# Optimization experiments

Hardware: AMD Instinct MI355X
Metric: run time of the kernel (lower is better)

Reference implementation:

```python
import jax, jax.numpy as jnp
import numpy as np

N = 4096          # batch of anchors
D = 128           # embedding dim
M = 4             # instances per class (balanced batch) -> 3 positives per anchor
MARGIN = 1.0
INF = jnp.float32(1e30)


def setup_inputs() -> dict:
    key = jax.random.key(0)
    inputs = jax.random.normal(key, (N, D), dtype=jnp.float32)
    targets = (jnp.arange(N, dtype=jnp.int32) // M).astype(jnp.int32)
    return {"inputs": inputs, "targets": targets}


def _forward(inputs, targets, key):
    n = inputs.shape[0]
    k_pos = M - 1            # positives per anchor (and multinomial draw count)
    k_neg = n - M            # negatives per anchor

    # euclidean_dist: ||xi||^2 + ||xj||^2 - 2 xi.xj, clamped and sqrt'ed
    sq = jnp.sum(inputs * inputs, axis=1)
    dist = sq[:, None] + sq[None, :] - 2.0 * (inputs @ inputs.T)
    dist = jnp.sqrt(jnp.clip(dist, 1e-12, None))

    same = targets[:, None] == targets[None, :]
    eye = jnp.eye(n, dtype=bool)
    pos_mask = same & ~eye
    neg_mask = ~same

    # balanced batch -> exactly k_pos positives / k_neg negatives per row;
    # push non-members to +inf and sort (original sorts pos/neg pairs anyway)
    pos_sorted = jnp.sort(jnp.where(pos_mask, dist, INF), axis=1)[:, :k_pos]  # [n, 3]
    neg_sorted = jnp.sort(jnp.where(neg_mask, dist, INF), axis=1)[:, :k_neg]  # [n, n-M]

    pos3 = pos_sorted[:, :3]  # pos_pair[:3]

    # GaussDistribution over the (sorted) negative row
    neg_mean = jnp.mean(neg_sorted, axis=1, keepdims=True)
    neg_std = jnp.sqrt(jnp.mean((neg_sorted - neg_mean) ** 2, axis=1, keepdims=True))
    # prob = exp((x-mean)^2 / (2 std^2)); use log-weights for Gumbel-top-k
    log_prob = (neg_sorted - neg_mean) ** 2 / (2.0 * neg_std ** 2)

    # multinomial without replacement == top-k of log_prob + Gumbel noise
    g = jax.random.gumbel(key, neg_sorted.shape, dtype=jnp.float32)
    _, idx = jax.lax.top_k(log_prob + g, k_pos)                 # [n, 3]
    sampled = jnp.take_along_axis(neg_sorted, idx, axis=1)      # [n, 3]

    # masked_select(neg_pair < pos_pair[-1] + 0.05) -> boolean keep mask
    kept = sampled < (pos3[:, -1:] + 0.05)
    cnt = jnp.sum(kept, axis=1)
    any_kept = cnt > 0

    # pos_loss = 0.5*mean(log(1+exp(-2*(margin - pos))))
    pos_loss = 0.5 * jnp.mean(jax.nn.softplus(-2.0 * (MARGIN - pos3)), axis=1)
    # neg_loss = 0.05*mean over kept of log(1+exp(20*(margin - neg)))
    neg_terms = jax.nn.softplus(20.0 * (MARGIN - sampled))
    neg_loss = 0.05 * jnp.sum(jnp.where(kept, neg_terms, 0.0), axis=1) / jnp.maximum(cnt, 1)

    row_loss = jnp.where(any_kept, pos_loss + neg_loss, 0.0)
    loss = jnp.sum(row_loss) / n

    # err: pos_pair[0] < neg_pair[0] - 0.1 (first kept sampled negative)
    first_idx = jnp.argmax(kept, axis=1)
    neg0 = jnp.take_along_axis(sampled, first_idx[:, None], axis=1)[:, 0]
    err = jnp.sum((any_kept & (pos3[:, 0] < neg0 - 0.1)).astype(jnp.float32))
    prec = 1.0 - err / n

    pos_d = jnp.mean(pos_sorted)
    neg_d = jnp.mean(neg_sorted)
    return loss, prec, pos_d, neg_d


def reference(inputs, targets):
    key = jax.random.key(42)  # fixed sampling key (torch.multinomial analogue)
    return _forward(inputs, targets, key)
```

## Files before the change

### kernel.cpp

```cpp
#include <hip/hip_runtime.h>
#include <stdint.h>

#define NROW 4096
#define NDIM 128
#define KNEG 4092
#define INF_VAL 1e30f
#define BUCKETS 2048
#define GTOT ((size_t)NROW * (size_t)KNEG)
#define DISTBLKS 1024
#define DSTR 68

typedef __attribute__((ext_vector_type(8))) short short8;
typedef __attribute__((ext_vector_type(4))) float f32x4;

__device__ __forceinline__ uint32_t rotl32(uint32_t v, int d) {
  return __builtin_rotateleft32(v, (unsigned)d);
}

__device__ __forceinline__ void threefry2x32(uint32_t x0, uint32_t x1,
                                             uint32_t& y0, uint32_t& y1) {
  const uint32_t k0 = 0u, k1 = 42u;
  const uint32_t k2 = 0x1BD11BDAu ^ k0 ^ k1;
  uint32_t v0 = x0 + k0, v1 = x1 + k1;
#define TF_R(r) v0 += v1; v1 = rotl32(v1, r); v1 ^= v0;
  TF_R(13) TF_R(15) TF_R(26) TF_R(6)
  v0 += k1; v1 += k2 + 1u;
  TF_R(17) TF_R(29) TF_R(16) TF_R(24)
  v0 += k2; v1 += k0 + 2u;
  TF_R(13) TF_R(15) TF_R(26) TF_R(6)
  v0 += k0; v1 += k1 + 3u;
  TF_R(17) TF_R(29) TF_R(16) TF_R(24)
  v0 += k1; v1 += k2 + 4u;
  TF_R(13) TF_R(15) TF_R(26) TF_R(6)
  v0 += k2; v1 += k0 + 5u;
#undef TF_R
  y0 = v0; y1 = v1;
}

__device__ __forceinline__ float gumbel_ref(uint32_t f) {
  uint32_t y0, y1;
  threefry2x32(0u, f, y0, y1);
  uint32_t m = y1 >> 9;
  float fm = (float)m;
  float nl = fmaf(-0.69314718f, __log2f(fm), 15.942385f);
  if (m == 0u) nl = 87.33655f;
  return -0.69314718f * __log2f(nl);
}

__device__ __forceinline__ float softplus_ref(float x) {
  return fmaxf(x, 0.0f) + log1pf(expf(-fabsf(x)));
}

__device__ __forceinline__ ushort f2h(float f) {
  _Float16 h = (_Float16)f;
  return *(ushort*)&h;
}
__device__ __forceinline__ float h2f(ushort u) {
  _Float16 h = *(_Float16*)&u;
  return (float)h;
}
__device__ __forceinline__ float bf2f(ushort u) {
  return __uint_as_float(((uint32_t)u) << 16);
}
__device__ __forceinline__ ushort f2bf(float f) {
  uint32_t u = __float_as_uint(f);
  u += 0x7fffu + ((u >> 16) & 1u);
  return (ushort)(u >> 16);
}

__device__ __forceinline__ int bucket_code(ushort code) {
  return min(max((int)code - 0x4000, 0), BUCKETS - 1);
}

__global__ __launch_bounds__(64) void prep_kernel(const float* __restrict__ X,
                                                  float* __restrict__ sq,
                                                  ushort* __restrict__ Xbf) {
  int i = blockIdx.x;
  int lane = threadIdx.x;
  float2 v = ((const float2*)(X + (size_t)i * NDIM))[lane];
  float s = v.x * v.x + v.y * v.y;
  for (int o = 32; o > 0; o >>= 1) s += __shfl_down(s, o);
  if (lane == 0) sq[i] = s;
  ushort2 h;
  h.x = f2bf(v.x);
  h.y = f2bf(v.y);
  ((ushort2*)(Xbf + (size_t)i * NDIM))[lane] = h;
}

__global__ __launch_bounds__(256) void dist_gumbel(const ushort* __restrict__ Xbf,
                                                   const float* __restrict__ sq,
                                                   ushort* __restrict__ distb,
                                                   ushort* __restrict__ gh) {
  __shared__ ushort Als[128 * DSTR];
  __shared__ ushort Bls[128 * DSTR];
  const int tid = threadIdx.x;
  const int bi = blockIdx.x >> 5, bj = blockIdx.x & 31;
  const int wave = tid >> 6, lane = tid & 63;
  const int q = lane >> 4, ln = lane & 15;
  const ushort* Ag = Xbf + (size_t)bi * 128 * NDIM;
  const ushort* Bg = Xbf + (size_t)bj * 128 * NDIM;

  f32x4 acc[8][2];
#pragma unroll
  for (int mt = 0; mt < 8; ++mt)
#pragma unroll
    for (int nt = 0; nt < 2; ++nt) acc[mt][nt] = (f32x4){0.f, 0.f, 0.f, 0.f};

  for (int kh = 0; kh < 2; ++kh) {
    if (kh) __syncthreads();
#pragma unroll
    for (int t = 0; t < 4; ++t) {
      int c = tid + 256 * t;
      int r = c >> 3, k8 = (c & 7) << 3;
      *(short8*)&Als[r * DSTR + k8] =
          *(const short8*)(Ag + (size_t)r * NDIM + kh * 64 + k8);
      *(short8*)&Bls[r * DSTR + k8] =
          *(const short8*)(Bg + (size_t)r * NDIM + kh * 64 + k8);
    }
    __syncthreads();
#pragma unroll
    for (int k0 = 0; k0 < 64; k0 += 32) {
      int kf = k0 + q * 8;
      short8 a[8], b[2];
#pragma unroll
      for (int mt = 0; mt < 8; ++mt)
        a[mt] = *(const short8*)&Als[(mt * 16 + ln) * DSTR + kf];
#pragma unroll
      for (int nt = 0; nt < 2; ++nt)
        b[nt] = *(const short8*)&Bls[(wave * 32 + 2 * ln + nt) * DSTR + kf];
#pragma unroll
      for (int mt = 0; mt < 8; ++mt)
#pragma unroll
        for (int nt = 0; nt < 2; ++nt)
          acc[mt][nt] = __builtin_amdgcn_mfma_f32_16x16x32_bf16(
              a[mt], b[nt], acc[mt][nt], 0, 0, 0);
    }
  }

  const int jcol = bj * 128 + wave * 32 + 2 * ln;
  float sqj0 = sq[jcol], sqj1 = sq[jcol + 1];
#pragma unroll
  for (int mt = 0; mt < 8; ++mt) {
    int ibase = bi * 128 + mt * 16 + q * 4;
#pragma unroll
    for (int r = 0; r < 4; ++r) {
      int i = ibase + r;
      float sqi = sq[i];
      float dx = sqrtf(fmaxf(sqi + sqj0 - 2.0f * acc[mt][0][r], 1e-12f));
      float dy = sqrtf(fmaxf(sqi + sqj1 - 2.0f * acc[mt][1][r], 1e-12f));
      uint32_t pack = ((uint32_t)f2bf(dy) << 16) | (uint32_t)f2bf(dx);
      *(uint32_t*)(distb + (size_t)i * NROW + jcol) = pack;
    }
  }

  if (gh) {
    uint32_t b0 = (uint32_t)blockIdx.x * 16368u;
#pragma unroll
    for (int t = 0; t < 16; ++t) {
      int c = tid + 256 * t;
      if (c < 4092) {
        uint32_t f0 = b0 + (uint32_t)c * 4u;
        ushort4 h;
        h.x = f2h(gumbel_ref(f0 + 0u));
        h.y = f2h(gumbel_ref(f0 + 1u));
        h.z = f2h(gumbel_ref(f0 + 2u));
        h.w = f2h(gumbel_ref(f0 + 3u));
        *(ushort4*)(gh + f0) = h;
      }
    }
  }
}

__global__ __launch_bounds__(256) void row_kernel(const ushort* __restrict__ distb,
                                                  const ushort* __restrict__ Gh,
                                                  float4* __restrict__ part) {
  __shared__ alignas(16) ushort sortc[NROW];
  __shared__ alignas(16) int base[BUCKETS];
  __shared__ float wredf[8];
  __shared__ int wtot[4];
  __shared__ float s_pos[3];
  __shared__ float s_sel[3];

  float* cscore = (float*)base;
  float* cx     = (float*)base + 768;
  int*   crank  = (int*)sortc;
  float* redf   = (float*)((char*)sortc + 3072);
  int*   redi   = (int*)((char*)sortc + 4096);
  int*   redi2  = (int*)((char*)sortc + 5120);

  const int i = blockIdx.x;
  const int tid = threadIdx.x;
  const int lane = tid & 63, wid = tid >> 6;
  const ushort* row = distb + (size_t)i * NROW;
  const int gbase = i & ~3;

  {
    int4* b4 = (int4*)base;
    b4[tid] = (int4){0, 0, 0, 0};
    b4[tid + 256] = (int4){0, 0, 0, 0};
  }

  ushort cd[16];
  float x[16];
  {
    short8 r0 = *(const short8*)(row + tid * 16);
    short8 r1 = *(const short8*)(row + tid * 16 + 8);
#pragma unroll
    for (int k = 0; k < 8; ++k) {
      cd[k] = (ushort)r0[k];     x[k] = bf2f(cd[k]);
      cd[8 + k] = (ushort)r1[k]; x[8 + k] = bf2f(cd[8 + k]);
    }
  }

  if (tid == (gbase >> 4)) {
    float p[3]; int np = 0;
#pragma unroll
    for (int qq = 0; qq < 4; ++qq) {
      int j = gbase + qq;
      if (j != i) p[np++] = x[j & 15];
    }
    float a = p[0], b = p[1], c = p[2], t_;
    if (a > b) { t_ = a; a = b; b = t_; }
    if (b > c) { t_ = b; b = c; c = t_; }
    if (a > b) { t_ = a; a = b; b = t_; }
    s_pos[0] = a; s_pos[1] = b; s_pos[2] = c;
  }

#pragma unroll
  for (int qq = 0; qq < 16; ++qq) {
    int j = tid * 16 + qq;
    if ((j >> 2) == (i >> 2)) { x[qq] = INF_VAL; cd[qq] = 0x7F80u; }
  }
  __syncthreads();

  int bkt[16];
  int ord[16];
  float ls = 0.f;
#pragma unroll
  for (int qq = 0; qq < 16; ++qq) {
    bkt[qq] = bucket_code(cd[qq]);
    ord[qq] = atomicAdd(&base[bkt[qq]], 1);
    if (x[qq] < 1e29f) ls += x[qq];
  }
  for (int o = 32; o > 0; o >>= 1) ls += __shfl_down(ls, o);
  if (lane == 0) wredf[wid] = ls;
  __syncthreads();
  const float negsum = wredf[0] + wredf[1] + wredf[2] + wredf[3];
  const float mean = negsum / (float)KNEG;

  int c8[8]; int lsum = 0;
#pragma unroll
  for (int qq = 0; qq < 8; ++qq) {
    int t_ = base[tid * 8 + qq];
    c8[qq] = lsum; lsum += t_;
  }
  float ls2 = 0.f;
#pragma unroll
  for (int qq = 0; qq < 16; ++qq)
    if (x[qq] < 1e29f) { float z = x[qq] - mean; ls2 += z * z; }
  int incl = lsum;
  for (int off = 1; off < 64; off <<= 1) {
    int o = __shfl_up(incl, off);
    if (lane >= off) incl += o;
  }
  for (int o = 32; o > 0; o >>= 1) ls2 += __shfl_down(ls2, o);
  if (lane == 63) wtot[wid] = incl;
  if (lane == 0) wredf[4 + wid] = ls2;
  __syncthreads();
  const float var = (wredf[4] + wredf[5] + wredf[6] + wredf[7]) / (float)KNEG;
  const float stdv = sqrtf(var);
  const float rdenom = __frcp_rn(2.0f * stdv * stdv);
  int excl = incl - lsum;
#pragma unroll
  for (int w = 0; w < 4; ++w) if (w < wid) excl += wtot[w];
#pragma unroll
  for (int qq = 0; qq < 8; ++qq) base[tid * 8 + qq] = excl + c8[qq];
  __syncthreads();

#pragma unroll
  for (int qq = 0; qq < 16; ++qq) {
    int p = base[bkt[qq]] + ord[qq];
    sortc[p] = cd[qq];
  }
  __syncthreads();

  const uint32_t fbase = (uint32_t)i * (uint32_t)KNEG;
  const ushort* grow = Gh ? (Gh + fbase) : nullptr;
  ushort gcode[16];
  if (grow) {
#pragma unroll
    for (int qq = 0; qq < 16; ++qq) gcode[qq] = grow[tid + 256 * qq];
  }

  float t0s = -1e38f, t1s = -1e38f, t2s = -1e38f;
  int   t0r = 0x7fffffff, t1r = 0x7fffffff, t2r = 0x7fffffff;
  float t0x = 0.f, t1x = 0.f, t2x = 0.f;
#pragma unroll
  for (int qq = 0; qq < 16; ++qq) {
    int p = tid + 256 * qq;
    float xv = bf2f(sortc[p]);
    if (p < KNEG) {
      float z = xv - mean;
      float gv = grow ? h2f(gcode[qq]) : gumbel_ref(fbase + (uint32_t)p);
      float sv = fmaf(z * z, rdenom, gv);
      if (sv > t2s || (sv == t2s && p < t2r)) {
        t2s = sv; t2r = p; t2x = xv;
        if (t2s > t1s || (t2s == t1s && t2r < t1r)) {
          float ts = t1s; int tr = t1r; float tx = t1x;
          t1s = t2s; t1r = t2r; t1x = t2x; t2s = ts; t2r = tr; t2x = tx;
        }
        if (t1s > t0s || (t1s == t0s && t1r < t0r)) {
          float ts = t0s; int tr = t0r; float tx = t0x;
          t0s = t1s; t0r = t1r; t0x = t1x; t1s = ts; t1r = tr; t1x = tx;
        }
      }
    }
  }
  __syncthreads();

  cscore[tid * 3 + 0] = t0s; crank[tid * 3 + 0] = t0r; cx[tid * 3 + 0] = t0x;
  cscore[tid * 3 + 1] = t1s; crank[tid * 3 + 1] = t1r; cx[tid * 3 + 1] = t1x;
  cscore[tid * 3 + 2] = t2s; crank[tid * 3 + 2] = t2r; cx[tid * 3 + 2] = t2x;
  __syncthreads();

  for (int t = 0; t < 3; ++t) {
    float bs = -1e38f; int br = 0x7fffffff; int bidx = 0;
    for (int k = tid; k < 768; k += 256) {
      float s_ = cscore[k]; int r_ = crank[k];
      if (s_ > bs || (s_ == bs && r_ < br)) { bs = s_; br = r_; bidx = k; }
    }
    redf[tid] = bs; redi[tid] = br; redi2[tid] = bidx;
    __syncthreads();
    if (tid < 64) {
      float s0_ = redf[tid]; int r0_ = redi[tid]; int i0_ = redi2[tid];
#pragma unroll
      for (int o = 64; o < 256; o += 64) {
        float s1 = redf[tid + o]; int r1 = redi[tid + o];
        if (s1 > s0_ || (s1 == s0_ && r1 < r0_)) {
          s0_ = s1; r0_ = r1; i0_ = redi2[tid + o];
        }
      }
      for (int off = 32; off > 0; off >>= 1) {
        float s1 = __shfl_down(s0_, off);
        int r1 = __shfl_down(r0_, off);
        int i1 = __shfl_down(i0_, off);
        if (s1 > s0_ || (s1 == s0_ && r1 < r0_)) { s0_ = s1; r0_ = r1; i0_ = i1; }
      }
      if (tid == 0) { s_sel[t] = cx[i0_]; cscore[i0_] = -1e38f; }
    }
    __syncthreads();
  }

  if (tid == 0) {
    float p0 = s_pos[0], p1 = s_pos[1], p2 = s_pos[2];
    float thr = p2 + 0.05f;
    float samp[3]; bool kept[3]; int cnt = 0;
#pragma unroll
    for (int t = 0; t < 3; ++t) {
      samp[t] = s_sel[t];
      kept[t] = samp[t] < thr;
      cnt += kept[t] ? 1 : 0;
    }
    bool any = cnt > 0;
    float pos_loss = 0.5f *
        (softplus_ref(-2.0f * (1.0f - p0)) + softplus_ref(-2.0f * (1.0f - p1)) +
         softplus_ref(-2.0f * (1.0f - p2))) / 3.0f;
    float nsum = 0.0f;
#pragma unroll
    for (int t = 0; t < 3; ++t)
      if (kept[t]) nsum += softplus_ref(20.0f * (1.0f - samp[t]));
    float neg_loss = 0.05f * nsum / (float)(cnt > 0 ? cnt : 1);
    float row_loss = any ? (pos_loss + neg_loss) : 0.0f;
    int first = kept[0] ? 0 : (kept[1] ? 1 : (kept[2] ? 2 : 0));
    float neg0 = samp[first];
    float errv = (any && (p0 < neg0 - 0.1f)) ? 1.0f : 0.0f;
    float4 pr;
    pr.x = row_loss; pr.y = errv; pr.z = p0 + p1 + p2; pr.w = negsum;
    part[i] = pr;
  }
}

__global__ __launch_bounds__(256) void reduce_kernel(const float4* __restrict__ part,
                                                     float* __restrict__ out) {
  __shared__ double wsum[4][4];
  const int tid = threadIdx.x;
  const int lane = tid & 63, wid = tid >> 6;
  double s0 = 0.0, s1 = 0.0, s2 = 0.0, s3 = 0.0;
  for (int k = tid; k < NROW; k += 256) {
    float4 v = part[k];
    s0 += (double)v.x; s1 += (double)v.y; s2 += (double)v.z; s3 += (double)v.w;
  }
  for (int o = 32; o > 0; o >>= 1) {
    s0 += __shfl_down(s0, o); s1 += __shfl_down(s1, o);
    s2 += __shfl_down(s2, o); s3 += __shfl_down(s3, o);
  }
  if (lane == 0) {
    wsum[wid][0] = s0; wsum[wid][1] = s1; wsum[wid][2] = s2; wsum[wid][3] = s3;
  }
  __syncthreads();
  if (tid == 0) {
    double a0 = wsum[0][0] + wsum[1][0] + wsum[2][0] + wsum[3][0];
    double a1 = wsum[0][1] + wsum[1][1] + wsum[2][1] + wsum[3][1];
    double a2 = wsum[0][2] + wsum[1][2] + wsum[2][2] + wsum[3][2];
    double a3 = wsum[0][3] + wsum[1][3] + wsum[2][3] + wsum[3][3];
    out[0] = (float)(a0 / (double)NROW);
    out[1] = (float)(1.0 - a1 / (double)NROW);
    out[2] = (float)(a2 / ((double)NROW * 3.0));
    out[3] = (float)(a3 / ((double)NROW * (double)KNEG));
  }
}

extern "C" void kernel_launch(void* const* d_in, const int* in_sizes, int n_in,
                              void* d_out, int out_size, void* d_ws, size_t ws_size,
                              hipStream_t stream) {
  (void)in_sizes; (void)n_in; (void)out_size;
  const float* X = (const float*)d_in[0];
  float* out = (float*)d_out;
  char* ws = (char*)d_ws;

  ushort* distb = (ushort*)ws;
  size_t off = (size_t)NROW * NROW * sizeof(ushort);
  float* sq = (float*)(ws + off);            off += NROW * sizeof(float);
  ushort* Xbf = (ushort*)(ws + off);         off += (size_t)NROW * NDIM * sizeof(ushort);
  float4* part = (float4*)(ws + off);        off += (size_t)NROW * sizeof(float4);
  ushort* Gh = nullptr;
  if (ws_size >= off + GTOT * sizeof(ushort)) Gh = (ushort*)(ws + off);

  prep_kernel<<<NROW, 64, 0, stream>>>(X, sq, Xbf);
  dist_gumbel<<<DISTBLKS, 256, 0, stream>>>(Xbf, sq, distb, Gh);
  row_kernel<<<NROW, 256, 0, stream>>>(distb, Gh, part);
  reduce_kernel<<<1, 256, 0, stream>>>(part, out);
}
```

Baseline: 172.0 us.

## Skip scatter pass in row counting sort, fuse final reduce via last-block

The row kernel no longer scatters bucket codes into a sorted shared array. Each element keeps its bucket and in-bucket offset packed in registers, so its sorted rank comes from the prefix-summed bucket starts and is used directly to index Gumbel noise that is staged once into shared memory. The histogram is split into two copies, one per half-wave, to reduce atomic contention. The separate reduce kernel is folded into the row kernel through a last-block-done atomic counter, and prep now runs four rows per 256-thread block. Together these remove one barrier and scatter pass, one launch and some LDS traffic, at the cost of extra shared memory and atomic fences.

```diff
diff --git a/kernel.cpp b/kernel.cpp
--- a/kernel.cpp
+++ b/kernel.cpp
@@ -72,11 +72,13 @@
   return min(max((int)code - 0x4000, 0), BUCKETS - 1);
 }
 
-__global__ __launch_bounds__(64) void prep_kernel(const float* __restrict__ X,
-                                                  float* __restrict__ sq,
-                                                  ushort* __restrict__ Xbf) {
-  int i = blockIdx.x;
-  int lane = threadIdx.x;
+__global__ __launch_bounds__(256) void prep_kernel(const float* __restrict__ X,
+                                                   float* __restrict__ sq,
+                                                   ushort* __restrict__ Xbf,
+                                                   uint32_t* __restrict__ cnt) {
+  const int tid = threadIdx.x;
+  const int lane = tid & 63;
+  const int i = (blockIdx.x << 2) + (tid >> 6);
   float2 v = ((const float2*)(X + (size_t)i * NDIM))[lane];
   float s = v.x * v.x + v.y * v.y;
   for (int o = 32; o > 0; o >>= 1) s += __shfl_down(s, o);
@@ -85,6 +87,7 @@
   h.x = f2bf(v.x);
   h.y = f2bf(v.y);
   ((ushort2*)(Xbf + (size_t)i * NDIM))[lane] = h;
+  if (blockIdx.x == 0 && tid == 0) *cnt = 0u;
 }
 
 __global__ __launch_bounds__(256) void dist_gumbel(const ushort* __restrict__ Xbf,
@@ -173,20 +176,27 @@
 
 __global__ __launch_bounds__(256) void row_kernel(const ushort* __restrict__ distb,
                                                   const ushort* __restrict__ Gh,
-                                                  float4* __restrict__ part) {
-  __shared__ alignas(16) ushort sortc[NROW];
-  __shared__ alignas(16) int base[BUCKETS];
+                                                  float4* __restrict__ part,
+                                                  uint32_t* __restrict__ cnt,
+                                                  float* __restrict__ out) {
+  __shared__ alignas(16) int baseA[BUCKETS];
+  __shared__ alignas(16) int baseB_raw[BUCKETS + 16];
+  __shared__ alignas(16) ushort Gls[4096];
   __shared__ float wredf[8];
   __shared__ int wtot[4];
   __shared__ float s_pos[3];
   __shared__ float s_sel[3];
-
-  float* cscore = (float*)base;
-  float* cx     = (float*)base + 768;
-  int*   crank  = (int*)sortc;
-  float* redf   = (float*)((char*)sortc + 3072);
-  int*   redi   = (int*)((char*)sortc + 4096);
-  int*   redi2  = (int*)((char*)sortc + 5120);
+  __shared__ int s_last;
+  __shared__ double dsum[4][4];
+
+  int* baseB = baseB_raw + 16;
+
+  float* cscore = (float*)baseA;
+  float* cx     = (float*)baseA + 768;
+  int*   crank  = (int*)Gls;
+  float* redf   = (float*)((char*)Gls + 3072);
+  int*   redi   = (int*)((char*)Gls + 4096);
+  int*   redi2  = (int*)((char*)Gls + 5120);
 
   const int i = blockIdx.x;
   const int tid = threadIdx.x;
@@ -195,9 +205,11 @@
   const int gbase = i & ~3;
 
   {
-    int4* b4 = (int4*)base;
-    b4[tid] = (int4){0, 0, 0, 0};
-    b4[tid + 256] = (int4){0, 0, 0, 0};
+    int4 z4 = (int4){0, 0, 0, 0};
+    int4* za = (int4*)baseA;
+    za[tid] = z4; za[tid + 256] = z4;
+    int4* zb = (int4*)baseB;
+    zb[tid] = z4; zb[tid + 256] = z4;
   }
 
   ushort cd[16];
@@ -212,6 +224,18 @@
     }
   }
 
+  const uint32_t fbase = (uint32_t)i * (uint32_t)KNEG;
+  const ushort* grow = Gh ? (Gh + (size_t)fbase) : nullptr;
+  if (grow) {
+    const uint32_t* g4 = (const uint32_t*)grow;
+    uint32_t* gl = (uint32_t*)Gls;
+#pragma unroll
+    for (int t = 0; t < 8; ++t) {
+      int c = tid + 256 * t;
+      if (c < (KNEG / 2)) gl[c] = g4[c];
+    }
+  }
+
   if (tid == (gbase >> 4)) {
     float p[3]; int np = 0;
 #pragma unroll
@@ -233,13 +257,14 @@
   }
   __syncthreads();
 
-  int bkt[16];
-  int ord[16];
+  int pk[16];
+  int* hist = (lane & 32) ? baseB : baseA;
   float ls = 0.f;
 #pragma unroll
   for (int qq = 0; qq < 16; ++qq) {
-    bkt[qq] = bucket_code(cd[qq]);
-    ord[qq] = atomicAdd(&base[bkt[qq]], 1);
+    int b = bucket_code(cd[qq]);
+    int o = atomicAdd(&hist[b], 1);
+    pk[qq] = b | (o << 11);
     if (x[qq] < 1e29f) ls += x[qq];
   }
   for (int o = 32; o > 0; o >>= 1) ls += __shfl_down(ls, o);
@@ -248,12 +273,17 @@
   const float negsum = wredf[0] + wredf[1] + wredf[2] + wredf[3];
   const float mean = negsum / (float)KNEG;
 
+  int4 a0 = ((const int4*)baseA)[2 * tid];
+  int4 a1 = ((const int4*)baseA)[2 * tid + 1];
+  int4 b0 = ((const int4*)baseB)[2 * tid];
+  int4 b1 = ((const int4*)baseB)[2 * tid + 1];
+  int cA[8] = {a0.x, a0.y, a0.z, a0.w, a1.x, a1.y, a1.z, a1.w};
+  int tot[8] = {a0.x + b0.x, a0.y + b0.y, a0.z + b0.z, a0.w + b0.w,
+                a1.x + b1.x, a1.y + b1.y, a1.z + b1.z, a1.w + b1.w};
   int c8[8]; int lsum = 0;
 #pragma unroll
-  for (int qq = 0; qq < 8; ++qq) {
-    int t_ = base[tid * 8 + qq];
-    c8[qq] = lsum; lsum += t_;
-  }
+  for (int qq = 0; qq < 8; ++qq) { c8[qq] = lsum; lsum += tot[qq]; }
+
   float ls2 = 0.f;
 #pragma unroll
   for (int qq = 0; qq < 16; ++qq)
@@ -273,35 +303,30 @@
   int excl = incl - lsum;
 #pragma unroll
   for (int w = 0; w < 4; ++w) if (w < wid) excl += wtot[w];
-#pragma unroll
-  for (int qq = 0; qq < 8; ++qq) base[tid * 8 + qq] = excl + c8[qq];
-  __syncthreads();
-
-#pragma unroll
-  for (int qq = 0; qq < 16; ++qq) {
-    int p = base[bkt[qq]] + ord[qq];
-    sortc[p] = cd[qq];
-  }
-  __syncthreads();
-
-  const uint32_t fbase = (uint32_t)i * (uint32_t)KNEG;
-  const ushort* grow = Gh ? (Gh + fbase) : nullptr;
-  ushort gcode[16];
-  if (grow) {
-#pragma unroll
-    for (int qq = 0; qq < 16; ++qq) gcode[qq] = grow[tid + 256 * qq];
-  }
-
+  ((int4*)baseA)[2 * tid] =
+      (int4){excl + c8[0], excl + c8[1], excl + c8[2], excl + c8[3]};
+  ((int4*)baseA)[2 * tid + 1] =
+      (int4){excl + c8[4], excl + c8[5], excl + c8[6], excl + c8[7]};
+  ((int4*)baseB)[2 * tid] =
+      (int4){excl + c8[0] + cA[0], excl + c8[1] + cA[1],
+             excl + c8[2] + cA[2], excl + c8[3] + cA[3]};
+  ((int4*)baseB)[2 * tid + 1] =
+      (int4){excl + c8[4] + cA[4], excl + c8[5] + cA[5],
+             excl + c8[6] + cA[6], excl + c8[7] + cA[7]};
+  __syncthreads();
+
+  const int* startp = (lane & 32) ? baseB : baseA;
   float t0s = -1e38f, t1s = -1e38f, t2s = -1e38f;
   int   t0r = 0x7fffffff, t1r = 0x7fffffff, t2r = 0x7fffffff;
   float t0x = 0.f, t1x = 0.f, t2x = 0.f;
 #pragma unroll
   for (int qq = 0; qq < 16; ++qq) {
-    int p = tid + 256 * qq;
-    float xv = bf2f(sortc[p]);
-    if (p < KNEG) {
+    if (x[qq] < 1e29f) {
+      int b = pk[qq] & 2047;
+      int p = startp[b] + (pk[qq] >> 11);
+      float xv = x[qq];
       float z = xv - mean;
-      float gv = grow ? h2f(gcode[qq]) : gumbel_ref(fbase + (uint32_t)p);
+      float gv = grow ? h2f(Gls[p]) : gumbel_ref(fbase + (uint32_t)p);
       float sv = fmaf(z * z, rdenom, gv);
       if (sv > t2s || (sv == t2s && p < t2r)) {
         t2s = sv; t2r = p; t2x = xv;
@@ -354,14 +379,14 @@
   if (tid == 0) {
     float p0 = s_pos[0], p1 = s_pos[1], p2 = s_pos[2];
     float thr = p2 + 0.05f;
-    float samp[3]; bool kept[3]; int cnt = 0;
+    float samp[3]; bool kept[3]; int cntk = 0;
 #pragma unroll
     for (int t = 0; t < 3; ++t) {
       samp[t] = s_sel[t];
       kept[t] = samp[t] < thr;
-      cnt += kept[t] ? 1 : 0;
-    }
-    bool any = cnt > 0;
+      cntk += kept[t] ? 1 : 0;
+    }
+    bool any = cntk > 0;
     float pos_loss = 0.5f *
         (softplus_ref(-2.0f * (1.0f - p0)) + softplus_ref(-2.0f * (1.0f - p1)) +
          softplus_ref(-2.0f * (1.0f - p2))) / 3.0f;
@@ -369,44 +394,53 @@
 #pragma unroll
     for (int t = 0; t < 3; ++t)
       if (kept[t]) nsum += softplus_ref(20.0f * (1.0f - samp[t]));
-    float neg_loss = 0.05f * nsum / (float)(cnt > 0 ? cnt : 1);
+    float neg_loss = 0.05f * nsum / (float)(cntk > 0 ? cntk : 1);
     float row_loss = any ? (pos_loss + neg_loss) : 0.0f;
     int first = kept[0] ? 0 : (kept[1] ? 1 : (kept[2] ? 2 : 0));
     float neg0 = samp[first];
     float errv = (any && (p0 < neg0 - 0.1f)) ? 1.0f : 0.0f;
-    float4 pr;
-    pr.x = row_loss; pr.y = errv; pr.z = p0 + p1 + p2; pr.w = negsum;
-    part[i] = pr;
-  }
-}
-
-__global__ __launch_bounds__(256) void reduce_kernel(const float4* __restrict__ part,
-                                                     float* __restrict__ out) {
-  __shared__ double wsum[4][4];
-  const int tid = threadIdx.x;
-  const int lane = tid & 63, wid = tid >> 6;
-  double s0 = 0.0, s1 = 0.0, s2 = 0.0, s3 = 0.0;
-  for (int k = tid; k < NROW; k += 256) {
-    float4 v = part[k];
-    s0 += (double)v.x; s1 += (double)v.y; s2 += (double)v.z; s3 += (double)v.w;
-  }
-  for (int o = 32; o > 0; o >>= 1) {
-    s0 += __shfl_down(s0, o); s1 += __shfl_down(s1, o);
-    s2 += __shfl_down(s2, o); s3 += __shfl_down(s3, o);
-  }
-  if (lane == 0) {
-    wsum[wid][0] = s0; wsum[wid][1] = s1; wsum[wid][2] = s2; wsum[wid][3] = s3;
-  }
-  __syncthreads();
-  if (tid == 0) {
-    double a0 = wsum[0][0] + wsum[1][0] + wsum[2][0] + wsum[3][0];
-    double a1 = wsum[0][1] + wsum[1][1] + wsum[2][1] + wsum[3][1];
-    double a2 = wsum[0][2] + wsum[1][2] + wsum[2][2] + wsum[3][2];
-    double a3 = wsum[0][3] + wsum[1][3] + wsum[2][3] + wsum[3][3];
-    out[0] = (float)(a0 / (double)NROW);
-    out[1] = (float)(1.0 - a1 / (double)NROW);
-    out[2] = (float)(a2 / ((double)NROW * 3.0));
-    out[3] = (float)(a3 / ((double)NROW * (double)KNEG));
+
+    float* pf = (float*)(part + i);
+    __hip_atomic_store(pf + 0, row_loss, __ATOMIC_RELAXED, __HIP_MEMORY_SCOPE_AGENT);
+    __hip_atomic_store(pf + 1, errv, __ATOMIC_RELAXED, __HIP_MEMORY_SCOPE_AGENT);
+    __hip_atomic_store(pf + 2, p0 + p1 + p2, __ATOMIC_RELAXED, __HIP_MEMORY_SCOPE_AGENT);
+    __hip_atomic_store(pf + 3, negsum, __ATOMIC_RELAXED, __HIP_MEMORY_SCOPE_AGENT);
+    __threadfence();
+    uint32_t tk = __hip_atomic_fetch_add(cnt, 1u, __ATOMIC_ACQ_REL,
+                                         __HIP_MEMORY_SCOPE_AGENT);
+    s_last = (tk == (uint32_t)(NROW - 1)) ? 1 : 0;
+  }
+  __syncthreads();
+
+  if (s_last) {
+    __threadfence();
+    double s0 = 0.0, s1 = 0.0, s2 = 0.0, s3 = 0.0;
+    const float* pf = (const float*)part;
+    for (int k = tid; k < NROW; k += 256) {
+      float vx = __hip_atomic_load(pf + 4 * k + 0, __ATOMIC_RELAXED, __HIP_MEMORY_SCOPE_AGENT);
+      float vy = __hip_atomic_load(pf + 4 * k + 1, __ATOMIC_RELAXED, __HIP_MEMORY_SCOPE_AGENT);
+      float vz = __hip_atomic_load(pf + 4 * k + 2, __ATOMIC_RELAXED, __HIP_MEMORY_SCOPE_AGENT);
+      float vw = __hip_atomic_load(pf + 4 * k + 3, __ATOMIC_RELAXED, __HIP_MEMORY_SCOPE_AGENT);
+      s0 += (double)vx; s1 += (double)vy; s2 += (double)vz; s3 += (double)vw;
+    }
+    for (int o = 32; o > 0; o >>= 1) {
+      s0 += __shfl_down(s0, o); s1 += __shfl_down(s1, o);
+      s2 += __shfl_down(s2, o); s3 += __shfl_down(s3, o);
+    }
+    if (lane == 0) {
+      dsum[wid][0] = s0; dsum[wid][1] = s1; dsum[wid][2] = s2; dsum[wid][3] = s3;
+    }
+    __syncthreads();
+    if (tid == 0) {
+      double a0 = dsum[0][0] + dsum[1][0] + dsum[2][0] + dsum[3][0];
+      double a1 = dsum[0][1] + dsum[1][1] + dsum[2][1] + dsum[3][1];
+      double a2 = dsum[0][2] + dsum[1][2] + dsum[2][2] + dsum[3][2];
+      double a3 = dsum[0][3] + dsum[1][3] + dsum[2][3] + dsum[3][3];
+      out[0] = (float)(a0 / (double)NROW);
+      out[1] = (float)(1.0 - a1 / (double)NROW);
+      out[2] = (float)(a2 / ((double)NROW * 3.0));
+      out[3] = (float)(a3 / ((double)NROW * (double)KNEG));
+    }
   }
 }
 
@@ -423,11 +457,11 @@
   float* sq = (float*)(ws + off);            off += NROW * sizeof(float);
   ushort* Xbf = (ushort*)(ws + off);         off += (size_t)NROW * NDIM * sizeof(ushort);
   float4* part = (float4*)(ws + off);        off += (size_t)NROW * sizeof(float4);
+  uint32_t* cnt = (uint32_t*)(ws + off);     off += 16;
   ushort* Gh = nullptr;
   if (ws_size >= off + GTOT * sizeof(ushort)) Gh = (ushort*)(ws + off);
 
-  prep_kernel<<<NROW, 64, 0, stream>>>(X, sq, Xbf);
+  prep_kernel<<<NROW / 4, 256, 0, stream>>>(X, sq, Xbf, cnt);
   dist_gumbel<<<DISTBLKS, 256, 0, stream>>>(Xbf, sq, distb, Gh);
-  row_kernel<<<NROW, 256, 0, stream>>>(distb, Gh, part);
-  reduce_kernel<<<1, 256, 0, stream>>>(part, out);
-}
+  row_kernel<<<NROW, 256, 0, stream>>>(distb, Gh, part, cnt, out);
+}
```

New measurement: 300.6 us. 1.75x slower.

## Exploit distance matrix symmetry: compute upper-triangle tiles and mirror via LDS transpose

Applied to the files above, without the earlier changes.

The distance GEMM now computes only the 528 upper-triangular 128x128 tiles and writes the transposed tile through shared memory for off-diagonal blocks, roughly halving the MFMA work. The Gumbel generation still runs over all 1024 blocks, so the extra blocks do only noise work. The prep kernel also packs four rows per 256-thread block to cut the launch block count. The cost is a serial loop to decode the tile index, an extra LDS transpose pass with a barrier, and possible bank conflicts from the 130-element row stride.

```diff
diff --git a/kernel.cpp b/kernel.cpp
--- a/kernel.cpp
+++ b/kernel.cpp
@@ -8,7 +8,9 @@
 #define BUCKETS 2048
 #define GTOT ((size_t)NROW * (size_t)KNEG)
 #define DISTBLKS 1024
+#define NTILEP 528
 #define DSTR 68
+#define TSTR 130
 
 typedef __attribute__((ext_vector_type(8))) short short8;
 typedef __attribute__((ext_vector_type(4))) float f32x4;
@@ -72,11 +74,12 @@
   return min(max((int)code - 0x4000, 0), BUCKETS - 1);
 }
 
-__global__ __launch_bounds__(64) void prep_kernel(const float* __restrict__ X,
-                                                  float* __restrict__ sq,
-                                                  ushort* __restrict__ Xbf) {
-  int i = blockIdx.x;
-  int lane = threadIdx.x;
+__global__ __launch_bounds__(256) void prep_kernel(const float* __restrict__ X,
+                                                   float* __restrict__ sq,
+                                                   ushort* __restrict__ Xbf) {
+  const int tid = threadIdx.x;
+  const int lane = tid & 63;
+  const int i = (blockIdx.x << 2) + (tid >> 6);
   float2 v = ((const float2*)(X + (size_t)i * NDIM))[lane];
   float s = v.x * v.x + v.y * v.y;
   for (int o = 32; o > 0; o >>= 1) s += __shfl_down(s, o);
@@ -94,62 +97,94 @@
   __shared__ ushort Als[128 * DSTR];
   __shared__ ushort Bls[128 * DSTR];
   const int tid = threadIdx.x;
-  const int bi = blockIdx.x >> 5, bj = blockIdx.x & 31;
   const int wave = tid >> 6, lane = tid & 63;
   const int q = lane >> 4, ln = lane & 15;
-  const ushort* Ag = Xbf + (size_t)bi * 128 * NDIM;
-  const ushort* Bg = Xbf + (size_t)bj * 128 * NDIM;
-
-  f32x4 acc[8][2];
-#pragma unroll
-  for (int mt = 0; mt < 8; ++mt)
-#pragma unroll
-    for (int nt = 0; nt < 2; ++nt) acc[mt][nt] = (f32x4){0.f, 0.f, 0.f, 0.f};
-
-  for (int kh = 0; kh < 2; ++kh) {
-    if (kh) __syncthreads();
-#pragma unroll
-    for (int t = 0; t < 4; ++t) {
-      int c = tid + 256 * t;
-      int r = c >> 3, k8 = (c & 7) << 3;
-      *(short8*)&Als[r * DSTR + k8] =
-          *(const short8*)(Ag + (size_t)r * NDIM + kh * 64 + k8);
-      *(short8*)&Bls[r * DSTR + k8] =
-          *(const short8*)(Bg + (size_t)r * NDIM + kh * 64 + k8);
-    }
+
+  if (blockIdx.x < NTILEP) {
+    int bi = 0, rem = blockIdx.x;
+    while (rem >= 32 - bi) { rem -= 32 - bi; ++bi; }
+    const int bj = bi + rem;
+
+    const ushort* Ag = Xbf + (size_t)bi * 128 * NDIM;
+    const ushort* Bg = Xbf + (size_t)bj * 128 * NDIM;
+
+    f32x4 acc[8][2];
+#pragma unroll
+    for (int mt = 0; mt < 8; ++mt)
+#pragma unroll
+      for (int nt = 0; nt < 2; ++nt) acc[mt][nt] = (f32x4){0.f, 0.f, 0.f, 0.f};
+
+    for (int kh = 0; kh < 2; ++kh) {
+      if (kh) __syncthreads();
+#pragma unroll
+      for (int t = 0; t < 4; ++t) {
+        int c = tid + 256 * t;
+        int r = c >> 3, k8 = (c & 7) << 3;
+        *(short8*)&Als[r * DSTR + k8] =
+            *(const short8*)(Ag + (size_t)r * NDIM + kh * 64 + k8);
+        *(short8*)&Bls[r * DSTR + k8] =
+            *(const short8*)(Bg + (size_t)r * NDIM + kh * 64 + k8);
+      }
+      __syncthreads();
+#pragma unroll
+      for (int k0 = 0; k0 < 64; k0 += 32) {
+        int kf = k0 + q * 8;
+        short8 a[8], b[2];
+#pragma unroll
+        for (int mt = 0; mt < 8; ++mt)
+          a[mt] = *(const short8*)&Als[(mt * 16 + ln) * DSTR + kf];
+#pragma unroll
+        for (int nt = 0; nt < 2; ++nt)
+          b[nt] = *(const short8*)&Bls[(wave * 32 + 2 * ln + nt) * DSTR + kf];
+#pragma unroll
+        for (int mt = 0; mt < 8; ++mt)
+#pragma unroll
+          for (int nt = 0; nt < 2; ++nt)
+            acc[mt][nt] = __builtin_amdgcn_mfma_f32_16x16x32_bf16(
+                a[mt], b[nt], acc[mt][nt], 0, 0, 0);
+      }
+    }
+
     __syncthreads();
-#pragma unroll
-    for (int k0 = 0; k0 < 64; k0 += 32) {
-      int kf = k0 + q * 8;
-      short8 a[8], b[2];
-#pragma unroll
-      for (int mt = 0; mt < 8; ++mt)
-        a[mt] = *(const short8*)&Als[(mt * 16 + ln) * DSTR + kf];
-#pragma unroll
-      for (int nt = 0; nt < 2; ++nt)
-        b[nt] = *(const short8*)&Bls[(wave * 32 + 2 * ln + nt) * DSTR + kf];
-#pragma unroll
-      for (int mt = 0; mt < 8; ++mt)
-#pragma unroll
-        for (int nt = 0; nt < 2; ++nt)
-          acc[mt][nt] = __builtin_amdgcn_mfma_f32_16x16x32_bf16(
-              a[mt], b[nt], acc[mt][nt], 0, 0, 0);
-    }
-  }
-
-  const int jcol = bj * 128 + wave * 32 + 2 * ln;
-  float sqj0 = sq[jcol], sqj1 = sq[jcol + 1];
-#pragma unroll
-  for (int mt = 0; mt < 8; ++mt) {
-    int ibase = bi * 128 + mt * 16 + q * 4;
-#pragma unroll
-    for (int r = 0; r < 4; ++r) {
-      int i = ibase + r;
-      float sqi = sq[i];
-      float dx = sqrtf(fmaxf(sqi + sqj0 - 2.0f * acc[mt][0][r], 1e-12f));
-      float dy = sqrtf(fmaxf(sqi + sqj1 - 2.0f * acc[mt][1][r], 1e-12f));
-      uint32_t pack = ((uint32_t)f2bf(dy) << 16) | (uint32_t)f2bf(dx);
-      *(uint32_t*)(distb + (size_t)i * NROW + jcol) = pack;
+
+    const bool mirror = (bi != bj);
+    const int jl = wave * 32 + 2 * ln;
+    const int jcol = bj * 128 + jl;
+    float sqj0 = sq[jcol], sqj1 = sq[jcol + 1];
+    ushort* Tb = (jl < 64) ? Als : Bls;
+    const int trow = (jl & 63) * TSTR;
+#pragma unroll
+    for (int mt = 0; mt < 8; ++mt) {
+      int il0 = mt * 16 + q * 4;
+      int ibase = bi * 128 + il0;
+#pragma unroll
+      for (int r = 0; r < 4; ++r) {
+        int i = ibase + r;
+        float sqi = sq[i];
+        float dx = sqrtf(fmaxf(sqi + sqj0 - 2.0f * acc[mt][0][r], 1e-12f));
+        float dy = sqrtf(fmaxf(sqi + sqj1 - 2.0f * acc[mt][1][r], 1e-12f));
+        ushort cx_ = f2bf(dx), cy_ = f2bf(dy);
+        uint32_t pack = ((uint32_t)cy_ << 16) | (uint32_t)cx_;
+        *(uint32_t*)(distb + (size_t)i * NROW + jcol) = pack;
+        if (mirror) {
+          Tb[trow + il0 + r] = cx_;
+          Tb[trow + TSTR + il0 + r] = cy_;
+        }
+      }
+    }
+
+    if (mirror) {
+      __syncthreads();
+#pragma unroll
+      for (int t = 0; t < 32; ++t) {
+        int linear = tid + 256 * t;
+        int jr = linear >> 6;
+        int cp = linear & 63;
+        const ushort* Rb = (jr < 64) ? Als : Bls;
+        uint32_t pack = *(const uint32_t*)&Rb[(jr & 63) * TSTR + 2 * cp];
+        *(uint32_t*)(distb + (size_t)(bj * 128 + jr) * NROW + bi * 128 + 2 * cp) =
+            pack;
+      }
     }
   }
 
@@ -426,7 +461,7 @@
   ushort* Gh = nullptr;
   if (ws_size >= off + GTOT * sizeof(ushort)) Gh = (ushort*)(ws + off);
 
-  prep_kernel<<<NROW, 64, 0, stream>>>(X, sq, Xbf);
+  prep_kernel<<<NROW / 4, 256, 0, stream>>>(X, sq, Xbf);
   dist_gumbel<<<DISTBLKS, 256, 0, stream>>>(Xbf, sq, distb, Gh);
   row_kernel<<<NROW, 256, 0, stream>>>(distb, Gh, part);
   reduce_kernel<<<1, 256, 0, stream>>>(part, out);
```

Result: no change. 175.1 us (+1.8%).
